# Kernel tuning notes

Measured on AMD Instinct MI355X. Metric: run time of the kernel, lower is better.

The kernel has to match this reference:

```python
import jax, jax.numpy as jnp
import numpy as np
from jax import lax

B = 16
C = 80                      # num_classes
IMG = 1024                  # square input image (H = W)
STRIDES = (8, 16, 32, 64, 128)
FEAT = (128, 64, 32, 16, 8) # IMG / stride per FPN level
SCORE_THRESH = 0.2
NMS_THRESH = 0.6
TOPK = 1000                 # topk_candidates per level
DETS = 100                  # detections_per_img


def _make_anchors(fs, stride):
    # one anchor per location, width = height = stride, centered on the cell
    ys, xs = jnp.meshgrid(jnp.arange(fs, dtype=jnp.float32),
                          jnp.arange(fs, dtype=jnp.float32), indexing="ij")
    cx = (xs.reshape(-1) + 0.5) * stride
    cy = (ys.reshape(-1) + 0.5) * stride
    h = stride / 2.0
    return jnp.stack([cx - h, cy - h, cx + h, cy + h], axis=-1)


def setup_inputs() -> dict:
    key = jax.random.key(0)
    ks = jax.random.split(key, 15)
    inp = {}
    for l, (fs, st) in enumerate(zip(FEAT, STRIDES)):
        hw = fs * fs
        inp[f"cls{l}"] = jax.random.normal(ks[3 * l + 0], (B, hw, C), jnp.float32)
        inp[f"ctr{l}"] = jax.random.normal(ks[3 * l + 1], (B, hw, 1), jnp.float32)
        inp[f"reg{l}"] = jax.random.uniform(ks[3 * l + 2], (B, hw, 4), jnp.float32)
        inp[f"anc{l}"] = _make_anchors(fs, st)
    return inp


def _decode(rel, anc):
    # BoxLinearCoder.decode with normalize_by_size=True
    cx = (anc[..., 0] + anc[..., 2]) * 0.5
    cy = (anc[..., 1] + anc[..., 3]) * 0.5
    w = anc[..., 2] - anc[..., 0]
    h = anc[..., 3] - anc[..., 1]
    rel = rel * jnp.stack([w, h, w, h], axis=-1)
    return jnp.stack([cx - rel[..., 0], cy - rel[..., 1],
                      cx + rel[..., 2], cy + rel[..., 3]], axis=-1)


def _level_candidates(cls, ctr, reg, anc):
    # score = sqrt(sigmoid(cls) * sigmoid(ctrness)), per torchvision FCOS
    scores = jnp.sqrt(jax.nn.sigmoid(cls) * jax.nn.sigmoid(ctr))  # [B,HW,C]
    flat = scores.reshape(scores.shape[0], -1)                    # [B,HW*C]
    # emulate the score threshold with masking (invalid -> -1, sorts last)
    masked = jnp.where(flat > SCORE_THRESH, flat, -1.0)
    k = min(TOPK, flat.shape[1])
    top_s, top_i = lax.top_k(masked, k)                           # [B,k]
    a_idx = top_i // C
    labels = top_i % C
    reg_sel = jnp.take_along_axis(reg, a_idx[..., None], axis=1)  # [B,k,4]
    boxes = _decode(reg_sel, anc[a_idx])                          # [B,k,4]
    boxes = jnp.clip(boxes, 0.0, float(IMG))                      # clip to image
    return boxes, top_s, labels


def _nms_single(boxes, scores, labels):
    # class-batched greedy NMS on one image, fixed DETS output slots
    off = jnp.float32(IMG + 1)
    nb = boxes + (labels.astype(boxes.dtype) * off)[:, None]  # class offset trick
    areas = (nb[:, 2] - nb[:, 0]) * (nb[:, 3] - nb[:, 1])

    def body(i, carry):
        s, bo, so, lo = carry
        j = jnp.argmax(s)
        bo = bo.at[i].set(boxes[j])
        so = so.at[i].set(s[j])
        lo = lo.at[i].set(labels[j])
        bj = nb[j]
        xx1 = jnp.maximum(bj[0], nb[:, 0])
        yy1 = jnp.maximum(bj[1], nb[:, 1])
        xx2 = jnp.minimum(bj[2], nb[:, 2])
        yy2 = jnp.minimum(bj[3], nb[:, 3])
        inter = jnp.maximum(xx2 - xx1, 0.0) * jnp.maximum(yy2 - yy1, 0.0)
        iou = inter / (areas + areas[j] - inter + 1e-9)
        s = jnp.where(iou > NMS_THRESH, -jnp.inf, s)  # suppress (incl. j itself)
        return s, bo, so, lo

    init = (scores,
            jnp.zeros((DETS, 4), boxes.dtype),
            jnp.zeros((DETS,), scores.dtype),
            jnp.zeros((DETS,), labels.dtype))
    _, bo, so, lo = lax.fori_loop(0, DETS, body, init)
    valid = so > SCORE_THRESH
    bo = jnp.where(valid[:, None], bo, 0.0)
    so = jnp.where(valid, so, 0.0)
    lo = jnp.where(valid, lo, -1)
    return bo, so, lo


def reference(cls0, cls1, cls2, cls3, cls4,
              ctr0, ctr1, ctr2, ctr3, ctr4,
              reg0, reg1, reg2, reg3, reg4,
              anc0, anc1, anc2, anc3, anc4):
    clss = (cls0, cls1, cls2, cls3, cls4)
    ctrs = (ctr0, ctr1, ctr2, ctr3, ctr4)
    regs = (reg0, reg1, reg2, reg3, reg4)
    ancs = (anc0, anc1, anc2, anc3, anc4)
    all_b, all_s, all_l = [], [], []
    for cls, ctr, reg, anc in zip(clss, ctrs, regs, ancs):
        b, s, l = _level_candidates(cls, ctr, reg, anc)
        all_b.append(b); all_s.append(s); all_l.append(l)
    boxes = jnp.concatenate(all_b, axis=1)    # [B, sum_k, 4]
    scores = jnp.concatenate(all_s, axis=1)   # [B, sum_k]
    labels = jnp.concatenate(all_l, axis=1)   # [B, sum_k]
    return jax.vmap(_nms_single)(boxes, scores, labels)
```

## Files before the change

kernel.cpp:

```cpp
#include <hip/hip_runtime.h>
#include <stdint.h>

namespace {

constexpr int kB = 16;
constexpr int kC = 80;
constexpr int kNLev = 5;
constexpr int kTopK = 1000;
constexpr int kDets = 100;
constexpr int kNBins = 2048;
constexpr int kCap = 4096;
constexpr float kScoreT = 0.2f;
constexpr float kNmsT = 0.6f;
constexpr int kChunk = 16384;
constexpr int kHW[5] = {16384, 4096, 1024, 256, 64};
constexpr int kLvlOff[5] = {0, 16384, 20480, 21504, 21760};
constexpr int kHWTot = 21824;
constexpr int kNTot = kNLev * kTopK;
constexpr int kChunksPerImg = 108;

struct LvlPtrs {
  const float* reg[5];
  const float* anc[5];
};

struct ClsPtrs {
  const float* cls[5];
};

__device__ __forceinline__ float sigm(float x) {
  return 1.0f / (1.0f + expf(-x));
}

__device__ __forceinline__ void chunk_map(int c, int* L, int* ch) {
  if (c < 80)       { *L = 0; *ch = c; }
  else if (c < 100) { *L = 1; *ch = c - 80; }
  else if (c < 105) { *L = 2; *ch = c - 100; }
  else if (c < 107) { *L = 3; *ch = c - 105; }
  else              { *L = 4; *ch = 0; }
}

__global__ void ksigctr(const float* __restrict__ c0, const float* __restrict__ c1,
                        const float* __restrict__ c2, const float* __restrict__ c3,
                        const float* __restrict__ c4, float* __restrict__ sct) {
  int gid = blockIdx.x * blockDim.x + threadIdx.x;
  if (gid >= kB * kHWTot) return;
  int b = gid / kHWTot;
  int pa = gid - b * kHWTot;
  const float* src; int hw; int off;
  if (pa < 16384)      { src = c0; off = 0;     hw = 16384; }
  else if (pa < 20480) { src = c1; off = 16384; hw = 4096; }
  else if (pa < 21504) { src = c2; off = 20480; hw = 1024; }
  else if (pa < 21760) { src = c3; off = 21504; hw = 256; }
  else                 { src = c4; off = 21760; hw = 64; }
  sct[gid] = sigm(src[(size_t)b * hw + (pa - off)]);
}

__global__ void khist_all(ClsPtrs CP, const float* __restrict__ sct,
                          unsigned int* __restrict__ ghist) {
  const int b = blockIdx.x / kChunksPerImg;
  const int c = blockIdx.x % kChunksPerImg;
  int L, ch; chunk_map(c, &L, &ch);
  const int HW = 16384 >> (2 * L);
  const int N = HW * kC;
  const int start = ch * kChunk;
  const int end = (start + kChunk < N) ? (start + kChunk) : N;
  __shared__ unsigned int lh[kNBins];
  for (int i = threadIdx.x; i < kNBins; i += blockDim.x) lh[i] = 0;
  __syncthreads();
  const float* clsb = CP.cls[L] + (size_t)b * N;
  const float* sctb = sct + (size_t)b * kHWTot + kLvlOff[L];
  for (int e0 = start + threadIdx.x * 4; e0 < end; e0 += blockDim.x * 4) {
    float4 v = *reinterpret_cast<const float4*>(clsb + e0);
    float cv[4] = {v.x, v.y, v.z, v.w};
#pragma unroll
    for (int q = 0; q < 4; ++q) {
      int e = e0 + q;
      float st = sctb[e / kC];
      float sc = sqrtf(sigm(cv[q]) * st);
      if (sc > kScoreT) {
        int bin = (int)((sc - kScoreT) * 2560.0f);
        if (bin > kNBins - 1) bin = kNBins - 1;
        atomicAdd(&lh[bin], 1u);
      }
    }
  }
  __syncthreads();
  unsigned int* gh = ghist + (size_t)(b * kNLev + L) * kNBins;
  for (int i = threadIdx.x; i < kNBins; i += blockDim.x)
    if (lh[i]) atomicAdd(&gh[i], lh[i]);
}

__global__ void kcutoff(const unsigned int* __restrict__ ghist, int* __restrict__ cutoff) {
  const int g = blockIdx.x;
  const unsigned int* h = ghist + (size_t)g * kNBins;
  __shared__ unsigned int lh[kNBins];
  __shared__ unsigned int tsum[256];
  for (int i = threadIdx.x; i < kNBins; i += 256) lh[i] = h[i];
  __syncthreads();
  unsigned int s = 0;
  for (int k = 0; k < kNBins / 256; ++k) s += lh[threadIdx.x * (kNBins / 256) + k];
  tsum[threadIdx.x] = s;
  __syncthreads();
  if (threadIdx.x == 0) {
    unsigned int acc = 0;
    for (int t = 255; t >= 0; --t) {
      if (acc + tsum[t] >= (unsigned)kTopK) {
        int c = 0;
        for (int bin = t * 8 + 7; bin >= t * 8; --bin) {
          acc += lh[bin];
          if (acc >= (unsigned)kTopK) { c = bin; break; }
        }
        cutoff[g] = c;
        return;
      }
      acc += tsum[t];
    }
    cutoff[g] = 0;
  }
}

__global__ void kcompact_all(ClsPtrs CP, const float* __restrict__ sct,
                             const int* __restrict__ cutoff, unsigned int* __restrict__ cnt,
                             unsigned long long* __restrict__ cand) {
  const int b = blockIdx.x / kChunksPerImg;
  const int c = blockIdx.x % kChunksPerImg;
  int L, ch; chunk_map(c, &L, &ch);
  const int HW = 16384 >> (2 * L);
  const int N = HW * kC;
  const int start = ch * kChunk;
  const int end = (start + kChunk < N) ? (start + kChunk) : N;
  const int g = b * kNLev + L;
  const int cut = cutoff[g];
  const float* clsb = CP.cls[L] + (size_t)b * N;
  const float* sctb = sct + (size_t)b * kHWTot + kLvlOff[L];
  for (int e0 = start + threadIdx.x * 4; e0 < end; e0 += blockDim.x * 4) {
    float4 v = *reinterpret_cast<const float4*>(clsb + e0);
    float cv[4] = {v.x, v.y, v.z, v.w};
#pragma unroll
    for (int q = 0; q < 4; ++q) {
      int e = e0 + q;
      float st = sctb[e / kC];
      float sc = sqrtf(sigm(cv[q]) * st);
      if (sc > kScoreT) {
        int bin = (int)((sc - kScoreT) * 2560.0f);
        if (bin > kNBins - 1) bin = kNBins - 1;
        if (bin >= cut) {
          unsigned int slot = atomicAdd(&cnt[g], 1u);
          if (slot < (unsigned)kCap) {
            unsigned int inv = 0xFFFFFFu - (((unsigned)L << 21) | (unsigned)e);
            cand[(size_t)g * kCap + slot] =
                ((unsigned long long)__float_as_uint(sc) << 24) | inv;
          }
        }
      }
    }
  }
}

__global__ void __launch_bounds__(1024)
krankl(const unsigned long long* __restrict__ cand, const unsigned int* __restrict__ cnt,
       unsigned long long* __restrict__ lvlsorted) {
  const int g = blockIdx.x;
  const int l = g % kNLev;
  __shared__ unsigned long long s[kCap];
  unsigned int nu = cnt[g];
  const int n = (nu > (unsigned)kCap) ? kCap : (int)nu;
  for (int i = threadIdx.x; i < n; i += 1024)
    s[i] = cand[(size_t)g * kCap + i];
  __syncthreads();
  for (int p = n + (int)threadIdx.x; p < kTopK; p += 1024)
    lvlsorted[(size_t)g * kTopK + p] =
        (unsigned long long)(kNTot - (l * kTopK + p));
  for (int i = threadIdx.x; i < n; i += 1024) {
    const unsigned long long ki = s[i];
    int r = 0;
#pragma unroll 8
    for (int j = 0; j < n; ++j) r += (s[j] > ki) ? 1 : 0;
    if (r < kTopK) lvlsorted[(size_t)g * kTopK + r] = ki;
  }
}

__device__ __forceinline__ void decode_key(unsigned long long key, int b, const LvlPtrs& P,
                                           float4* box, int* label_out, float* score_out) {
  float sc = __uint_as_float((unsigned int)(key >> 24));
  *score_out = sc;
  if (!(sc > kScoreT)) { *box = make_float4(0.f, 0.f, 0.f, 0.f); *label_out = -1; return; }
  unsigned int pk = 0xFFFFFFu - (unsigned int)(key & 0xFFFFFFu);
  int l = pk >> 21;
  int idx = pk & 0x1FFFFF;
  int pos = idx / kC;
  int label = idx - pos * kC;
  int hw = 16384 >> (2 * l);
  const float* rg = P.reg[l] + ((size_t)b * hw + pos) * 4;
  const float* an = P.anc[l] + (size_t)pos * 4;
  float a0 = an[0], a1 = an[1], a2 = an[2], a3 = an[3];
  float cx = (a0 + a2) * 0.5f, cy = (a1 + a3) * 0.5f;
  float w = a2 - a0, h = a3 - a1;
  float x0 = cx - rg[0] * w, y0 = cy - rg[1] * h;
  float x1 = cx + rg[2] * w, y1 = cy + rg[3] * h;
  x0 = fminf(fmaxf(x0, 0.f), 1024.f);
  y0 = fminf(fmaxf(y0, 0.f), 1024.f);
  x1 = fminf(fmaxf(x1, 0.f), 1024.f);
  y1 = fminf(fmaxf(y1, 0.f), 1024.f);
  *box = make_float4(x0, y0, x1, y1);
  *label_out = label;
}

__global__ void krank(const unsigned long long* __restrict__ lvlsorted,
                      unsigned long long* __restrict__ skey,
                      float4* __restrict__ obox, LvlPtrs P) {
  int gid = blockIdx.x * blockDim.x + threadIdx.x;
  if (gid >= kB * kNTot) return;
  int b = gid / kNTot;
  int r0 = gid - b * kNTot;
  int a = r0 / kTopK, p = r0 - a * kTopK;
  const unsigned long long* base = lvlsorted + (size_t)b * kNTot;
  unsigned long long key = base[a * kTopK + p];
  int rank = p;
  for (int a2 = 0; a2 < kNLev; ++a2) {
    if (a2 == a) continue;
    const unsigned long long* lst = base + a2 * kTopK;
    int lo = 0, hi = kTopK;
    while (lo < hi) {
      int mid = (lo + hi) >> 1;
      if (lst[mid] > key) lo = mid + 1; else hi = mid;
    }
    rank += lo;
  }
  float4 box; int label; float sc;
  decode_key(key, b, P, &box, &label, &sc);
  float off = (sc > kScoreT) ? (float)label * 1025.0f : 0.0f;
  skey[(size_t)b * kNTot + rank] = key;
  obox[(size_t)b * kNTot + rank] =
      make_float4(box.x + off, box.y + off, box.z + off, box.w + off);
}

__global__ void __launch_bounds__(64)
knms(const unsigned long long* __restrict__ skey, const float4* __restrict__ obox,
     LvlPtrs P, float* __restrict__ out) {
  const int b = blockIdx.x;
  const int lane = threadIdx.x;
  __shared__ float4 kbox[kDets];
  __shared__ float karea[kDets];
  __shared__ unsigned long long kkey[kDets];
  const unsigned long long* keys = skey + (size_t)b * kNTot;
  const float4* boxes = obox + (size_t)b * kNTot;
  int nkept = 0;
  for (int base = 0; base < kNTot && nkept < kDets; base += 64) {
    int j = base + lane;
    unsigned long long key = (j < kNTot) ? keys[j] : 0ull;
    float sc = __uint_as_float((unsigned int)(key >> 24));
    bool scval = (j < kNTot) && (sc > kScoreT);
    if (__ballot(scval) == 0ull) break;
    float4 bx = make_float4(0.f, 0.f, 0.f, 0.f);
    if (scval) bx = boxes[j];
    float area = (bx.z - bx.x) * (bx.w - bx.y);
    bool alive = scval;
    for (int k = 0; k < nkept; ++k) {
      float4 kb = kbox[k];
      float xx1 = fmaxf(kb.x, bx.x), yy1 = fmaxf(kb.y, bx.y);
      float xx2 = fminf(kb.z, bx.z), yy2 = fminf(kb.w, bx.w);
      float inter = fmaxf(xx2 - xx1, 0.f) * fmaxf(yy2 - yy1, 0.f);
      float iou = inter / (area + karea[k] - inter + 1e-9f);
      if (iou > kNmsT) alive = false;
    }
    unsigned long long mask = __ballot(alive);
    while (mask != 0ull && nkept < kDets) {
      int lead = (int)__builtin_ctzll(mask);
      float lx = __shfl(bx.x, lead);
      float ly = __shfl(bx.y, lead);
      float lz = __shfl(bx.z, lead);
      float lw = __shfl(bx.w, lead);
      float la = __shfl(area, lead);
      unsigned int khi = (unsigned int)__shfl((int)(key >> 32), lead);
      unsigned int klo = (unsigned int)__shfl((int)(key & 0xFFFFFFFFull), lead);
      if (lane == 0) {
        kbox[nkept] = make_float4(lx, ly, lz, lw);
        karea[nkept] = la;
        kkey[nkept] = (((unsigned long long)khi) << 32) | (unsigned long long)klo;
      }
      __syncthreads();
      ++nkept;
      float xx1 = fmaxf(lx, bx.x), yy1 = fmaxf(ly, bx.y);
      float xx2 = fminf(lz, bx.z), yy2 = fminf(lw, bx.w);
      float inter = fmaxf(xx2 - xx1, 0.f) * fmaxf(yy2 - yy1, 0.f);
      float iou = inter / (area + la - inter + 1e-9f);
      if (iou > kNmsT) alive = false;
      mask = __ballot(alive);
    }
  }
  for (int s = lane; s < kDets; s += 64) {
    float4 bo = make_float4(0.f, 0.f, 0.f, 0.f);
    float so = 0.f, lo = -1.f;
    if (s < nkept) {
      float4 box; int label; float sc;
      decode_key(kkey[s], b, P, &box, &label, &sc);
      bo = box; so = sc; lo = (float)label;
    }
    size_t bi = (size_t)b * kDets + s;
    out[bi * 4 + 0] = bo.x;
    out[bi * 4 + 1] = bo.y;
    out[bi * 4 + 2] = bo.z;
    out[bi * 4 + 3] = bo.w;
    out[(size_t)kB * kDets * 4 + bi] = so;
    out[(size_t)kB * kDets * 5 + bi] = lo;
  }
}

}

extern "C" void kernel_launch(void* const* d_in, const int* in_sizes, int n_in,
                              void* d_out, int out_size, void* d_ws, size_t ws_size,
                              hipStream_t stream) {
  ClsPtrs CP; LvlPtrs P;
  const float* ctr[5];
  for (int l = 0; l < 5; ++l) {
    CP.cls[l] = (const float*)d_in[4 * l + 0];
    ctr[l]    = (const float*)d_in[4 * l + 1];
    P.reg[l]  = (const float*)d_in[4 * l + 2];
    P.anc[l]  = (const float*)d_in[4 * l + 3];
  }

  char* w = (char*)d_ws;
  unsigned int* hist = (unsigned int*)w;          w += (size_t)80 * kNBins * 4;
  int* cutoff = (int*)w;                          w += 80 * 4;
  unsigned int* cnt = (unsigned int*)w;           w += 80 * 4;
  unsigned long long* cand = (unsigned long long*)w;      w += (size_t)80 * kCap * 8;
  unsigned long long* lvlsorted = (unsigned long long*)w; w += (size_t)80 * kTopK * 8;
  unsigned long long* skeyp = (unsigned long long*)w;     w += (size_t)kB * kNTot * 8;
  float4* oboxp = (float4*)w;                     w += (size_t)kB * kNTot * 16;
  float* sct = (float*)w;                         w += (size_t)kB * kHWTot * 4;

  hipMemsetAsync(hist, 0, (size_t)80 * kNBins * 4 + 80 * 8, stream);

  int sblocks = (kB * kHWTot + 255) / 256;
  ksigctr<<<sblocks, 256, 0, stream>>>(ctr[0], ctr[1], ctr[2], ctr[3], ctr[4], sct);

  khist_all<<<kB * kChunksPerImg, 256, 0, stream>>>(CP, sct, hist);

  kcutoff<<<80, 256, 0, stream>>>(hist, cutoff);

  kcompact_all<<<kB * kChunksPerImg, 256, 0, stream>>>(CP, sct, cutoff, cnt, cand);

  krankl<<<80, 1024, 0, stream>>>(cand, cnt, lvlsorted);

  int rblocks = (kB * kNTot + 255) / 256;
  krank<<<rblocks, 256, 0, stream>>>(lvlsorted, skeyp, oboxp, P);

  knms<<<kB, 64, 0, stream>>>(skeyp, oboxp, P, (float*)d_out);
}
```

Before: 240.2 us.

## Fuse centerness sigmoid into hist/compact kernels with LDS cache and smaller chunks

Removes the separate centerness-sigmoid kernel and its global scratch buffer. Each histogram and compaction block now computes the sigmoid of the centerness values it needs and caches them in shared memory. Chunk size is halved to give more blocks, and each thread processes 8 elements with two float4 loads. The cost is recomputing the centerness sigmoid in both passes and extra per-block setup.

```diff
diff --git a/kernel.cpp b/kernel.cpp
--- a/kernel.cpp
+++ b/kernel.cpp
@@ -12,12 +12,9 @@
 constexpr int kCap = 4096;
 constexpr float kScoreT = 0.2f;
 constexpr float kNmsT = 0.6f;
-constexpr int kChunk = 16384;
-constexpr int kHW[5] = {16384, 4096, 1024, 256, 64};
-constexpr int kLvlOff[5] = {0, 16384, 20480, 21504, 21760};
-constexpr int kHWTot = 21824;
+constexpr int kChunk = 8192;
 constexpr int kNTot = kNLev * kTopK;
-constexpr int kChunksPerImg = 108;
+constexpr int kChunksPerImg = 214;
 
 struct LvlPtrs {
   const float* reg[5];
@@ -26,6 +23,7 @@
 
 struct ClsPtrs {
   const float* cls[5];
+  const float* ctr[5];
 };
 
 __device__ __forceinline__ float sigm(float x) {
@@ -33,31 +31,15 @@
 }
 
 __device__ __forceinline__ void chunk_map(int c, int* L, int* ch) {
-  if (c < 80)       { *L = 0; *ch = c; }
-  else if (c < 100) { *L = 1; *ch = c - 80; }
-  else if (c < 105) { *L = 2; *ch = c - 100; }
-  else if (c < 107) { *L = 3; *ch = c - 105; }
+  if (c < 160)      { *L = 0; *ch = c; }
+  else if (c < 200) { *L = 1; *ch = c - 160; }
+  else if (c < 210) { *L = 2; *ch = c - 200; }
+  else if (c < 213) { *L = 3; *ch = c - 210; }
   else              { *L = 4; *ch = 0; }
 }
 
-__global__ void ksigctr(const float* __restrict__ c0, const float* __restrict__ c1,
-                        const float* __restrict__ c2, const float* __restrict__ c3,
-                        const float* __restrict__ c4, float* __restrict__ sct) {
-  int gid = blockIdx.x * blockDim.x + threadIdx.x;
-  if (gid >= kB * kHWTot) return;
-  int b = gid / kHWTot;
-  int pa = gid - b * kHWTot;
-  const float* src; int hw; int off;
-  if (pa < 16384)      { src = c0; off = 0;     hw = 16384; }
-  else if (pa < 20480) { src = c1; off = 16384; hw = 4096; }
-  else if (pa < 21504) { src = c2; off = 20480; hw = 1024; }
-  else if (pa < 21760) { src = c3; off = 21504; hw = 256; }
-  else                 { src = c4; off = 21760; hw = 64; }
-  sct[gid] = sigm(src[(size_t)b * hw + (pa - off)]);
-}
-
-__global__ void khist_all(ClsPtrs CP, const float* __restrict__ sct,
-                          unsigned int* __restrict__ ghist) {
+__global__ void __launch_bounds__(256)
+khist_all(ClsPtrs CP, unsigned int* __restrict__ ghist) {
   const int b = blockIdx.x / kChunksPerImg;
   const int c = blockIdx.x % kChunksPerImg;
   int L, ch; chunk_map(c, &L, &ch);
@@ -65,19 +47,27 @@
   const int N = HW * kC;
   const int start = ch * kChunk;
   const int end = (start + kChunk < N) ? (start + kChunk) : N;
+  const int locb = start / kC;
+  const int nloc = (end - 1) / kC - locb + 1;
   __shared__ unsigned int lh[kNBins];
-  for (int i = threadIdx.x; i < kNBins; i += blockDim.x) lh[i] = 0;
+  __shared__ float lsct[128];
+  for (int i = threadIdx.x; i < kNBins; i += 256) lh[i] = 0;
+  const float* ctrb = CP.ctr[L] + (size_t)b * HW;
+  for (int i = threadIdx.x; i < nloc; i += 256) lsct[i] = sigm(ctrb[locb + i]);
   __syncthreads();
   const float* clsb = CP.cls[L] + (size_t)b * N;
-  const float* sctb = sct + (size_t)b * kHWTot + kLvlOff[L];
-  for (int e0 = start + threadIdx.x * 4; e0 < end; e0 += blockDim.x * 4) {
-    float4 v = *reinterpret_cast<const float4*>(clsb + e0);
-    float cv[4] = {v.x, v.y, v.z, v.w};
+  for (int e0 = start + threadIdx.x * 8; e0 < end; e0 += 256 * 8) {
+    float4 v0 = *reinterpret_cast<const float4*>(clsb + e0);
+    float4 v1 = *reinterpret_cast<const float4*>(clsb + e0 + 4);
+    float f[8] = {v0.x, v0.y, v0.z, v0.w, v1.x, v1.y, v1.z, v1.w};
+    int loc0 = e0 / kC;
+    int c0 = e0 - loc0 * kC;
+    loc0 -= locb;
 #pragma unroll
-    for (int q = 0; q < 4; ++q) {
-      int e = e0 + q;
-      float st = sctb[e / kC];
-      float sc = sqrtf(sigm(cv[q]) * st);
+    for (int q = 0; q < 8; ++q) {
+      int cc = c0 + q;
+      float st = lsct[loc0 + (cc >= kC ? 1 : 0)];
+      float sc = sqrtf(sigm(f[q]) * st);
       if (sc > kScoreT) {
         int bin = (int)((sc - kScoreT) * 2560.0f);
         if (bin > kNBins - 1) bin = kNBins - 1;
@@ -87,7 +77,7 @@
   }
   __syncthreads();
   unsigned int* gh = ghist + (size_t)(b * kNLev + L) * kNBins;
-  for (int i = threadIdx.x; i < kNBins; i += blockDim.x)
+  for (int i = threadIdx.x; i < kNBins; i += 256)
     if (lh[i]) atomicAdd(&gh[i], lh[i]);
 }
 
@@ -120,9 +110,9 @@
   }
 }
 
-__global__ void kcompact_all(ClsPtrs CP, const float* __restrict__ sct,
-                             const int* __restrict__ cutoff, unsigned int* __restrict__ cnt,
-                             unsigned long long* __restrict__ cand) {
+__global__ void __launch_bounds__(256)
+kcompact_all(ClsPtrs CP, const int* __restrict__ cutoff, unsigned int* __restrict__ cnt,
+             unsigned long long* __restrict__ cand) {
   const int b = blockIdx.x / kChunksPerImg;
   const int c = blockIdx.x % kChunksPerImg;
   int L, ch; chunk_map(c, &L, &ch);
@@ -130,22 +120,32 @@
   const int N = HW * kC;
   const int start = ch * kChunk;
   const int end = (start + kChunk < N) ? (start + kChunk) : N;
+  const int locb = start / kC;
+  const int nloc = (end - 1) / kC - locb + 1;
+  __shared__ float lsct[128];
+  const float* ctrb = CP.ctr[L] + (size_t)b * HW;
+  for (int i = threadIdx.x; i < nloc; i += 256) lsct[i] = sigm(ctrb[locb + i]);
+  __syncthreads();
   const int g = b * kNLev + L;
   const int cut = cutoff[g];
   const float* clsb = CP.cls[L] + (size_t)b * N;
-  const float* sctb = sct + (size_t)b * kHWTot + kLvlOff[L];
-  for (int e0 = start + threadIdx.x * 4; e0 < end; e0 += blockDim.x * 4) {
-    float4 v = *reinterpret_cast<const float4*>(clsb + e0);
-    float cv[4] = {v.x, v.y, v.z, v.w};
+  for (int e0 = start + threadIdx.x * 8; e0 < end; e0 += 256 * 8) {
+    float4 v0 = *reinterpret_cast<const float4*>(clsb + e0);
+    float4 v1 = *reinterpret_cast<const float4*>(clsb + e0 + 4);
+    float f[8] = {v0.x, v0.y, v0.z, v0.w, v1.x, v1.y, v1.z, v1.w};
+    int loc0 = e0 / kC;
+    int c0 = e0 - loc0 * kC;
+    loc0 -= locb;
 #pragma unroll
-    for (int q = 0; q < 4; ++q) {
-      int e = e0 + q;
-      float st = sctb[e / kC];
-      float sc = sqrtf(sigm(cv[q]) * st);
+    for (int q = 0; q < 8; ++q) {
+      int cc = c0 + q;
+      float st = lsct[loc0 + (cc >= kC ? 1 : 0)];
+      float sc = sqrtf(sigm(f[q]) * st);
       if (sc > kScoreT) {
         int bin = (int)((sc - kScoreT) * 2560.0f);
         if (bin > kNBins - 1) bin = kNBins - 1;
         if (bin >= cut) {
+          int e = e0 + q;
           unsigned int slot = atomicAdd(&cnt[g], 1u);
           if (slot < (unsigned)kCap) {
             unsigned int inv = 0xFFFFFFu - (((unsigned)L << 21) | (unsigned)e);
@@ -314,10 +314,9 @@
                               void* d_out, int out_size, void* d_ws, size_t ws_size,
                               hipStream_t stream) {
   ClsPtrs CP; LvlPtrs P;
-  const float* ctr[5];
   for (int l = 0; l < 5; ++l) {
     CP.cls[l] = (const float*)d_in[4 * l + 0];
-    ctr[l]    = (const float*)d_in[4 * l + 1];
+    CP.ctr[l] = (const float*)d_in[4 * l + 1];
     P.reg[l]  = (const float*)d_in[4 * l + 2];
     P.anc[l]  = (const float*)d_in[4 * l + 3];
   }
@@ -330,18 +329,14 @@
   unsigned long long* lvlsorted = (unsigned long long*)w; w += (size_t)80 * kTopK * 8;
   unsigned long long* skeyp = (unsigned long long*)w;     w += (size_t)kB * kNTot * 8;
   float4* oboxp = (float4*)w;                     w += (size_t)kB * kNTot * 16;
-  float* sct = (float*)w;                         w += (size_t)kB * kHWTot * 4;
 
   hipMemsetAsync(hist, 0, (size_t)80 * kNBins * 4 + 80 * 8, stream);
 
-  int sblocks = (kB * kHWTot + 255) / 256;
-  ksigctr<<<sblocks, 256, 0, stream>>>(ctr[0], ctr[1], ctr[2], ctr[3], ctr[4], sct);
-
-  khist_all<<<kB * kChunksPerImg, 256, 0, stream>>>(CP, sct, hist);
+  khist_all<<<kB * kChunksPerImg, 256, 0, stream>>>(CP, hist);
 
   kcutoff<<<80, 256, 0, stream>>>(hist, cutoff);
 
-  kcompact_all<<<kB * kChunksPerImg, 256, 0, stream>>>(CP, sct, cutoff, cnt, cand);
+  kcompact_all<<<kB * kChunksPerImg, 256, 0, stream>>>(CP, cutoff, cnt, cand);
 
   krankl<<<80, 1024, 0, stream>>>(cand, cnt, lvlsorted);
 
```

Result: slower. 311.0 us (+29.5%).

## Fuse ctrness sigmoid into histogram/compact passes with per-block partial histograms

Applied to the files above, without the earlier changes.

Removes the separate centerness-sigmoid kernel and computes it inline from the raw ctr input in both the histogram and compaction passes. The histogram becomes coarser (512 bins) and each block writes its own partial histogram, which the cutoff kernel sums, so global atomics and the large memset go away. The loops are restructured to issue eight float4 loads before computing, and the hot path uses fast sigmoid, rcp and sqrt. The compaction pass filters on a slightly loosened fast-math threshold and recomputes exact scores for survivors. Candidate capacity grows to absorb the coarser bins, which risks more candidates reaching the rank kernel.

```diff
diff --git a/kernel.cpp b/kernel.cpp
--- a/kernel.cpp
+++ b/kernel.cpp
@@ -8,16 +8,15 @@
 constexpr int kNLev = 5;
 constexpr int kTopK = 1000;
 constexpr int kDets = 100;
-constexpr int kNBins = 2048;
-constexpr int kCap = 4096;
+constexpr int kNBins = 512;
+constexpr int kCap = 6144;
 constexpr float kScoreT = 0.2f;
 constexpr float kNmsT = 0.6f;
 constexpr int kChunk = 16384;
-constexpr int kHW[5] = {16384, 4096, 1024, 256, 64};
-constexpr int kLvlOff[5] = {0, 16384, 20480, 21504, 21760};
-constexpr int kHWTot = 21824;
 constexpr int kNTot = kNLev * kTopK;
 constexpr int kChunksPerImg = 108;
+constexpr int kLvlChunk0[5] = {0, 80, 100, 105, 107};
+constexpr int kLvlNChunk[5] = {80, 20, 5, 2, 1};
 
 struct LvlPtrs {
   const float* reg[5];
@@ -26,10 +25,14 @@
 
 struct ClsPtrs {
   const float* cls[5];
+  const float* ctr[5];
 };
 
 __device__ __forceinline__ float sigm(float x) {
   return 1.0f / (1.0f + expf(-x));
+}
+__device__ __forceinline__ float sigm_fast(float x) {
+  return __builtin_amdgcn_rcpf(1.0f + __expf(-x));
 }
 
 __device__ __forceinline__ void chunk_map(int c, int* L, int* ch) {
@@ -40,24 +43,8 @@
   else              { *L = 4; *ch = 0; }
 }
 
-__global__ void ksigctr(const float* __restrict__ c0, const float* __restrict__ c1,
-                        const float* __restrict__ c2, const float* __restrict__ c3,
-                        const float* __restrict__ c4, float* __restrict__ sct) {
-  int gid = blockIdx.x * blockDim.x + threadIdx.x;
-  if (gid >= kB * kHWTot) return;
-  int b = gid / kHWTot;
-  int pa = gid - b * kHWTot;
-  const float* src; int hw; int off;
-  if (pa < 16384)      { src = c0; off = 0;     hw = 16384; }
-  else if (pa < 20480) { src = c1; off = 16384; hw = 4096; }
-  else if (pa < 21504) { src = c2; off = 20480; hw = 1024; }
-  else if (pa < 21760) { src = c3; off = 21504; hw = 256; }
-  else                 { src = c4; off = 21760; hw = 64; }
-  sct[gid] = sigm(src[(size_t)b * hw + (pa - off)]);
-}
-
-__global__ void khist_all(ClsPtrs CP, const float* __restrict__ sct,
-                          unsigned int* __restrict__ ghist) {
+__global__ void __launch_bounds__(256)
+khist_all(ClsPtrs CP, unsigned int* __restrict__ ph) {
   const int b = blockIdx.x / kChunksPerImg;
   const int c = blockIdx.x % kChunksPerImg;
   int L, ch; chunk_map(c, &L, &ch);
@@ -66,63 +53,77 @@
   const int start = ch * kChunk;
   const int end = (start + kChunk < N) ? (start + kChunk) : N;
   __shared__ unsigned int lh[kNBins];
-  for (int i = threadIdx.x; i < kNBins; i += blockDim.x) lh[i] = 0;
+  for (int i = threadIdx.x; i < kNBins; i += 256) lh[i] = 0;
   __syncthreads();
   const float* clsb = CP.cls[L] + (size_t)b * N;
-  const float* sctb = sct + (size_t)b * kHWTot + kLvlOff[L];
-  for (int e0 = start + threadIdx.x * 4; e0 < end; e0 += blockDim.x * 4) {
-    float4 v = *reinterpret_cast<const float4*>(clsb + e0);
-    float cv[4] = {v.x, v.y, v.z, v.w};
-#pragma unroll
-    for (int q = 0; q < 4; ++q) {
-      int e = e0 + q;
-      float st = sctb[e / kC];
-      float sc = sqrtf(sigm(cv[q]) * st);
-      if (sc > kScoreT) {
-        int bin = (int)((sc - kScoreT) * 2560.0f);
-        if (bin > kNBins - 1) bin = kNBins - 1;
-        atomicAdd(&lh[bin], 1u);
+  const float* ctrb = CP.ctr[L] + (size_t)b * HW;
+  const int tid4 = (int)threadIdx.x * 4;
+#pragma unroll 1
+  for (int bb = 0; bb < 2; ++bb) {
+    const int base = start + bb * 8192;
+    float4 vf[8]; int ke[8]; bool kv[8];
+#pragma unroll
+    for (int k = 0; k < 8; ++k) {
+      int e = base + k * 1024 + tid4;
+      ke[k] = e; kv[k] = (e < end);
+      if (kv[k]) vf[k] = *reinterpret_cast<const float4*>(clsb + e);
+    }
+#pragma unroll
+    for (int k = 0; k < 8; ++k) {
+      if (!kv[k]) continue;
+      const int e = ke[k];
+      const int loc0 = (int)((unsigned)e / 80u);
+      const int c0 = e - loc0 * kC;
+      int loc1 = loc0 + 1; if (loc1 >= HW) loc1 = HW - 1;
+      const float st0 = sigm_fast(ctrb[loc0]);
+      const float st1 = sigm_fast(ctrb[loc1]);
+      const float f[4] = {vf[k].x, vf[k].y, vf[k].z, vf[k].w};
+#pragma unroll
+      for (int q = 0; q < 4; ++q) {
+        float st = (c0 + q >= kC) ? st1 : st0;
+        float sc = __builtin_amdgcn_sqrtf(sigm_fast(f[q]) * st);
+        int bin = (int)((sc - kScoreT) * 640.0f);
+        if (bin >= 0) {
+          if (bin > kNBins - 1) bin = kNBins - 1;
+          atomicAdd(&lh[bin], 1u);
+        }
       }
     }
   }
   __syncthreads();
-  unsigned int* gh = ghist + (size_t)(b * kNLev + L) * kNBins;
-  for (int i = threadIdx.x; i < kNBins; i += blockDim.x)
-    if (lh[i]) atomicAdd(&gh[i], lh[i]);
-}
-
-__global__ void kcutoff(const unsigned int* __restrict__ ghist, int* __restrict__ cutoff) {
+  unsigned int* dst = ph + (size_t)blockIdx.x * kNBins;
+  for (int i = threadIdx.x; i < kNBins; i += 256) dst[i] = lh[i];
+}
+
+__global__ void __launch_bounds__(256)
+kcutoff(const unsigned int* __restrict__ ph, int* __restrict__ cutoff) {
   const int g = blockIdx.x;
-  const unsigned int* h = ghist + (size_t)g * kNBins;
+  const int b = g / kNLev, L = g % kNLev;
+  const unsigned int* base =
+      ph + (size_t)(b * kChunksPerImg + kLvlChunk0[L]) * kNBins;
+  const int nb = kLvlNChunk[L];
   __shared__ unsigned int lh[kNBins];
-  __shared__ unsigned int tsum[256];
-  for (int i = threadIdx.x; i < kNBins; i += 256) lh[i] = h[i];
-  __syncthreads();
-  unsigned int s = 0;
-  for (int k = 0; k < kNBins / 256; ++k) s += lh[threadIdx.x * (kNBins / 256) + k];
-  tsum[threadIdx.x] = s;
+  unsigned int a0 = 0, a1 = 0;
+  for (int j = 0; j < nb; ++j) {
+    a0 += base[(size_t)j * kNBins + threadIdx.x];
+    a1 += base[(size_t)j * kNBins + 256 + threadIdx.x];
+  }
+  lh[threadIdx.x] = a0;
+  lh[256 + threadIdx.x] = a1;
   __syncthreads();
   if (threadIdx.x == 0) {
-    unsigned int acc = 0;
-    for (int t = 255; t >= 0; --t) {
-      if (acc + tsum[t] >= (unsigned)kTopK) {
-        int c = 0;
-        for (int bin = t * 8 + 7; bin >= t * 8; --bin) {
-          acc += lh[bin];
-          if (acc >= (unsigned)kTopK) { c = bin; break; }
-        }
-        cutoff[g] = c;
-        return;
-      }
-      acc += tsum[t];
-    }
-    cutoff[g] = 0;
-  }
-}
-
-__global__ void kcompact_all(ClsPtrs CP, const float* __restrict__ sct,
-                             const int* __restrict__ cutoff, unsigned int* __restrict__ cnt,
-                             unsigned long long* __restrict__ cand) {
+    unsigned int acc = 0; int cut = 0;
+    for (int bin = kNBins - 1; bin >= 0; --bin) {
+      acc += lh[bin];
+      if (acc >= (unsigned)kTopK) { cut = bin; break; }
+    }
+    cutoff[g] = cut;
+  }
+}
+
+__global__ void __launch_bounds__(256)
+kcompact_all(ClsPtrs CP, const int* __restrict__ cutoff, unsigned int* __restrict__ cnt,
+             unsigned long long* __restrict__ cand) {
   const int b = blockIdx.x / kChunksPerImg;
   const int c = blockIdx.x % kChunksPerImg;
   int L, ch; chunk_map(c, &L, &ch);
@@ -131,26 +132,49 @@
   const int start = ch * kChunk;
   const int end = (start + kChunk < N) ? (start + kChunk) : N;
   const int g = b * kNLev + L;
-  const int cut = cutoff[g];
+  float thr = kScoreT + (float)(cutoff[g] - 2) * (1.0f / 640.0f);
+  if (thr < 0.199f) thr = 0.199f;
   const float* clsb = CP.cls[L] + (size_t)b * N;
-  const float* sctb = sct + (size_t)b * kHWTot + kLvlOff[L];
-  for (int e0 = start + threadIdx.x * 4; e0 < end; e0 += blockDim.x * 4) {
-    float4 v = *reinterpret_cast<const float4*>(clsb + e0);
-    float cv[4] = {v.x, v.y, v.z, v.w};
-#pragma unroll
-    for (int q = 0; q < 4; ++q) {
-      int e = e0 + q;
-      float st = sctb[e / kC];
-      float sc = sqrtf(sigm(cv[q]) * st);
-      if (sc > kScoreT) {
-        int bin = (int)((sc - kScoreT) * 2560.0f);
-        if (bin > kNBins - 1) bin = kNBins - 1;
-        if (bin >= cut) {
-          unsigned int slot = atomicAdd(&cnt[g], 1u);
-          if (slot < (unsigned)kCap) {
-            unsigned int inv = 0xFFFFFFu - (((unsigned)L << 21) | (unsigned)e);
-            cand[(size_t)g * kCap + slot] =
-                ((unsigned long long)__float_as_uint(sc) << 24) | inv;
+  const float* ctrb = CP.ctr[L] + (size_t)b * HW;
+  unsigned long long* gc = cand + (size_t)g * kCap;
+  const int tid4 = (int)threadIdx.x * 4;
+#pragma unroll 1
+  for (int bb = 0; bb < 2; ++bb) {
+    const int base = start + bb * 8192;
+    float4 vf[8]; int ke[8]; bool kv[8];
+#pragma unroll
+    for (int k = 0; k < 8; ++k) {
+      int e = base + k * 1024 + tid4;
+      ke[k] = e; kv[k] = (e < end);
+      if (kv[k]) vf[k] = *reinterpret_cast<const float4*>(clsb + e);
+    }
+#pragma unroll
+    for (int k = 0; k < 8; ++k) {
+      if (!kv[k]) continue;
+      const int e = ke[k];
+      const int loc0 = (int)((unsigned)e / 80u);
+      const int c0 = e - loc0 * kC;
+      int loc1 = loc0 + 1; if (loc1 >= HW) loc1 = HW - 1;
+      const float t0 = ctrb[loc0];
+      const float t1 = ctrb[loc1];
+      const float st0 = sigm_fast(t0);
+      const float st1 = sigm_fast(t1);
+      const float f[4] = {vf[k].x, vf[k].y, vf[k].z, vf[k].w};
+#pragma unroll
+      for (int q = 0; q < 4; ++q) {
+        const bool hi = (c0 + q >= kC);
+        float st = hi ? st1 : st0;
+        float sa = __builtin_amdgcn_sqrtf(sigm_fast(f[q]) * st);
+        if (sa >= thr) {
+          float traw = hi ? t1 : t0;
+          float sex = sqrtf(sigm(f[q]) * sigm(traw));
+          if (sex > kScoreT) {
+            unsigned int slot = atomicAdd(&cnt[g], 1u);
+            if (slot < (unsigned)kCap) {
+              int ee = e + q;
+              unsigned int inv = 0xFFFFFFu - (((unsigned)L << 21) | (unsigned)ee);
+              gc[slot] = ((unsigned long long)__float_as_uint(sex) << 24) | inv;
+            }
           }
         }
       }
@@ -314,34 +338,31 @@
                               void* d_out, int out_size, void* d_ws, size_t ws_size,
                               hipStream_t stream) {
   ClsPtrs CP; LvlPtrs P;
-  const float* ctr[5];
   for (int l = 0; l < 5; ++l) {
     CP.cls[l] = (const float*)d_in[4 * l + 0];
-    ctr[l]    = (const float*)d_in[4 * l + 1];
+    CP.ctr[l] = (const float*)d_in[4 * l + 1];
     P.reg[l]  = (const float*)d_in[4 * l + 2];
     P.anc[l]  = (const float*)d_in[4 * l + 3];
   }
 
+  const int nblk = kB * kChunksPerImg;
+
   char* w = (char*)d_ws;
-  unsigned int* hist = (unsigned int*)w;          w += (size_t)80 * kNBins * 4;
+  unsigned int* ph = (unsigned int*)w;            w += (size_t)nblk * kNBins * 4;
   int* cutoff = (int*)w;                          w += 80 * 4;
   unsigned int* cnt = (unsigned int*)w;           w += 80 * 4;
   unsigned long long* cand = (unsigned long long*)w;      w += (size_t)80 * kCap * 8;
   unsigned long long* lvlsorted = (unsigned long long*)w; w += (size_t)80 * kTopK * 8;
   unsigned long long* skeyp = (unsigned long long*)w;     w += (size_t)kB * kNTot * 8;
   float4* oboxp = (float4*)w;                     w += (size_t)kB * kNTot * 16;
-  float* sct = (float*)w;                         w += (size_t)kB * kHWTot * 4;
-
-  hipMemsetAsync(hist, 0, (size_t)80 * kNBins * 4 + 80 * 8, stream);
-
-  int sblocks = (kB * kHWTot + 255) / 256;
-  ksigctr<<<sblocks, 256, 0, stream>>>(ctr[0], ctr[1], ctr[2], ctr[3], ctr[4], sct);
-
-  khist_all<<<kB * kChunksPerImg, 256, 0, stream>>>(CP, sct, hist);
-
-  kcutoff<<<80, 256, 0, stream>>>(hist, cutoff);
-
-  kcompact_all<<<kB * kChunksPerImg, 256, 0, stream>>>(CP, sct, cutoff, cnt, cand);
+
+  hipMemsetAsync(cutoff, 0, 80 * 8, stream);
+
+  khist_all<<<nblk, 256, 0, stream>>>(CP, ph);
+
+  kcutoff<<<80, 256, 0, stream>>>(ph, cutoff);
+
+  kcompact_all<<<nblk, 256, 0, stream>>>(CP, cutoff, cnt, cand);
 
   krankl<<<80, 1024, 0, stream>>>(cand, cnt, lvlsorted);
 
```

Result: slower. 276.7 us (+15.2%).
